# Kernel tuning notes

Hardware: AMD Instinct MI355X
Metric: run time of the kernel (lower is better)

The kernel has to match this reference:

```python
import jax, jax.numpy as jnp
import numpy as np

D_MODEL = 1024
N_HEAD = 16
HEAD_DIM = D_MODEL // N_HEAD
B, S = 4, 2048


def setup_inputs() -> dict:
    key = jax.random.key(0)
    ks = jax.random.split(key, 11)
    scale = 1.0 / np.sqrt(D_MODEL)
    inp = {
        "q": jax.random.normal(ks[0], (B, S, D_MODEL), jnp.float32),
        "k": jax.random.normal(ks[1], (B, S, D_MODEL), jnp.float32),
        "v": jax.random.normal(ks[2], (B, S, D_MODEL), jnp.float32),
        # torch nn.Linear weights: [out_features, in_features], y = x @ W.T + b
        "Wq": jax.random.normal(ks[3], (D_MODEL, D_MODEL), jnp.float32) * scale,
        "bq": jax.random.normal(ks[4], (D_MODEL,), jnp.float32) * scale,
        "Wk": jax.random.normal(ks[5], (D_MODEL, D_MODEL), jnp.float32) * scale,
        "bk": jax.random.normal(ks[6], (D_MODEL,), jnp.float32) * scale,
        "Wv": jax.random.normal(ks[7], (D_MODEL, D_MODEL), jnp.float32) * scale,
        "bv": jax.random.normal(ks[8], (D_MODEL,), jnp.float32) * scale,
        "Wo": jax.random.normal(ks[9], (D_MODEL, D_MODEL), jnp.float32) * scale,
        "bo": jax.random.normal(ks[10], (D_MODEL,), jnp.float32) * scale,
    }
    return inp


def _split_heads(x):
    # [B, S, D] -> [B, H, S, hd]
    b, s, _ = x.shape
    return x.reshape(b, s, N_HEAD, HEAD_DIM).transpose(0, 2, 1, 3)


def reference(q, k, v, Wq, bq, Wk, bk, Wv, bv, Wo, bo):
    qh = _split_heads(q @ Wq.T + bq)
    kh = _split_heads(k @ Wk.T + bk)
    vh = _split_heads(v @ Wv.T + bv)
    scores = jnp.einsum("bhqd,bhkd->bhqk", qh, kh) / jnp.sqrt(
        jnp.asarray(HEAD_DIM, qh.dtype)
    )
    weights = jax.nn.softmax(scores, axis=-1)  # [B, H, Sq, Sk]
    ctx = jnp.einsum("bhqk,bhkd->bhqd", weights, vh)
    b, h, s, d = ctx.shape
    ctx = ctx.transpose(0, 2, 1, 3).reshape(b, s, h * d)  # [B, S, D]
    return ctx @ Wo.T + bo
```

## Files before the change

### kernel.cpp

```cpp
#include <hip/hip_runtime.h>
#include <hip/hip_bf16.h>

typedef float   f32x4   __attribute__((ext_vector_type(4)));
typedef __bf16  bf16x8  __attribute__((ext_vector_type(8)));
typedef unsigned short u16x8 __attribute__((ext_vector_type(8)));
typedef unsigned short u16x4 __attribute__((ext_vector_type(4)));

#define DEVI __device__ __forceinline__

DEVI unsigned short f2bf_bits(float f) {
    __bf16 h = (__bf16)f;
    return __builtin_bit_cast(unsigned short, h);
}

DEVI f32x4 mfma_bf16(bf16x8 a, bf16x8 b, f32x4 c) {
    return __builtin_amdgcn_mfma_f32_16x16x32_bf16(a, b, c, 0, 0, 0);
}

DEVI float fast_exp2(float x) {
#if __has_builtin(__builtin_amdgcn_exp2f)
    return __builtin_amdgcn_exp2f(x);
#else
    float r;
    asm("v_exp_f32 %0, %1" : "=v"(r) : "v"(x));
    return r;
#endif
}

DEVI void gload16(const void* g, void* l) {
    __builtin_amdgcn_global_load_lds(
        (const __attribute__((address_space(1))) void*)g,
        (__attribute__((address_space(3))) void*)l, 16, 0, 0);
}

__global__ __launch_bounds__(256) void convert_w_kernel(
    const float* __restrict__ Wq, const float* __restrict__ Wk,
    const float* __restrict__ Wv, unsigned short* __restrict__ Wb)
{
    int idx = blockIdx.x * 256 + threadIdx.x;
    int which = idx >> 17;
    int off = (idx & 131071) * 8;
    const float* src = which == 0 ? Wq : (which == 1 ? Wk : Wv);
    f32x4 a = *(const f32x4*)(src + off);
    f32x4 b = *(const f32x4*)(src + off + 4);
    u16x8 h;
#pragma unroll
    for (int j = 0; j < 4; ++j) { h[j] = f2bf_bits(a[j]); h[4 + j] = f2bf_bits(b[j]); }
    *(u16x8*)(Wb + (size_t)which * 1048576 + off) = h;
}

template <bool A_ASYNC, bool OUT_F32>
__global__ __launch_bounds__(256) void gemm_bt_kernel(
    const void* __restrict__ Ap, const void* __restrict__ Wp,
    const float* __restrict__ bias, void* __restrict__ Cp,
    int M, int N, int K, float scale)
{
    __shared__ __align__(16) char ldsA[128 * 128];
    __shared__ __align__(16) char ldsB[128 * 128];
    const int t = threadIdx.x;
    const int wave = t >> 6, lane = t & 63;
    const int g = lane >> 4, c = lane & 15;
    const int rowbase = blockIdx.x * 128;
    const int colbase = blockIdx.y * 128;
    const int wr = (wave >> 1) * 64, wc = (wave & 1) * 64;

    const int arow = lane >> 3;
    const int aslot = (lane & 7) ^ arow;

    const float* fbase[4];
#pragma unroll
    for (int ch = 0; ch < 4; ++ch) {
        int id = ch * 256 + t;
        int row = id >> 3;
        int col = (id & 7) * 8;
        if constexpr (A_ASYNC)
            fbase[ch] = (const float*)Wp + (size_t)(colbase + row) * K + col;
        else
            fbase[ch] = (const float*)Ap + (size_t)(rowbase + row) * K + col;
    }

    f32x4 pre0[4], pre1[4];
#pragma unroll
    for (int ch = 0; ch < 4; ++ch) {
        pre0[ch] = *(const f32x4*)(fbase[ch]);
        pre1[ch] = *(const f32x4*)(fbase[ch] + 4);
    }

    f32x4 acc[4][4] = {};

    for (int kt = 0; kt < K; kt += 64) {
        if constexpr (A_ASYNC) {
            const unsigned short* Ab = (const unsigned short*)Ap;
#pragma unroll
            for (int j = 0; j < 4; ++j) {
                int rg = wave * 4 + j;
                int row = rg * 8 + arow;
                gload16(Ab + (size_t)(rowbase + row) * K + kt + aslot * 8,
                        ldsA + rg * 1024);
            }
        } else {
            const unsigned short* Wb = (const unsigned short*)Wp;
#pragma unroll
            for (int j = 0; j < 4; ++j) {
                int rg = wave * 4 + j;
                int row = rg * 8 + arow;
                gload16(Wb + (size_t)(colbase + row) * K + kt + aslot * 8,
                        ldsB + rg * 1024);
            }
        }

#pragma unroll
        for (int ch = 0; ch < 4; ++ch) {
            int id = ch * 256 + t;
            int row = id >> 3;
            int col = (id & 7) * 8;
            int dst = row * 128 + ((col * 2) ^ ((row & 7) << 4));
            u16x8 hv;
#pragma unroll
            for (int j = 0; j < 4; ++j) { hv[j] = f2bf_bits(pre0[ch][j]); hv[4 + j] = f2bf_bits(pre1[ch][j]); }
            if constexpr (A_ASYNC)
                *(u16x8*)(ldsB + dst) = hv;
            else
                *(u16x8*)(ldsA + dst) = hv;
        }
        __syncthreads();

        if (kt + 64 < K) {
#pragma unroll
            for (int ch = 0; ch < 4; ++ch) {
                pre0[ch] = *(const f32x4*)(fbase[ch] + kt + 64);
                pre1[ch] = *(const f32x4*)(fbase[ch] + kt + 68);
            }
        }

#pragma unroll
        for (int kk = 0; kk < 2; ++kk) {
            bf16x8 af[4], bfr[4];
#pragma unroll
            for (int i = 0; i < 4; ++i) {
                int ra = wr + i * 16 + c;
                af[i] = *(const bf16x8*)(ldsA + ra * 128 + ((kk * 64 + g * 16) ^ ((ra & 7) << 4)));
                int rb = wc + i * 16 + c;
                bfr[i] = *(const bf16x8*)(ldsB + rb * 128 + ((kk * 64 + g * 16) ^ ((rb & 7) << 4)));
            }
#pragma unroll
            for (int i = 0; i < 4; ++i)
#pragma unroll
                for (int j = 0; j < 4; ++j)
                    acc[i][j] = mfma_bf16(af[i], bfr[j], acc[i][j]);
        }
        __syncthreads();
    }

#pragma unroll
    for (int j = 0; j < 4; ++j) {
        int coln = colbase + wc + j * 16 + c;
        float bv = bias[coln];
#pragma unroll
        for (int i = 0; i < 4; ++i) {
            int row0 = rowbase + wr + i * 16 + g * 4;
#pragma unroll
            for (int r = 0; r < 4; ++r) {
                float val = (acc[i][j][r] + bv) * scale;
                if constexpr (OUT_F32)
                    ((float*)Cp)[(size_t)(row0 + r) * N + coln] = val;
                else
                    ((unsigned short*)Cp)[(size_t)(row0 + r) * N + coln] = f2bf_bits(val);
            }
        }
    }
}

__global__ __launch_bounds__(256) void transpose_v_kernel(
    const unsigned short* __restrict__ Vp, unsigned short* __restrict__ Vt)
{
    __shared__ unsigned short tile[64][72];
    const int t = threadIdx.x;
    const int bh = blockIdx.y, b = bh >> 4, h = bh & 15;
    const int s0 = blockIdx.x * 64;
#pragma unroll
    for (int ch = 0; ch < 2; ++ch) {
        int id = ch * 256 + t;
        int srow = id >> 3, dcol = (id & 7) * 8;
        u16x8 v = *(const u16x8*)(Vp + (size_t)(b * 2048 + s0 + srow) * 1024 + h * 64 + dcol);
        *(u16x8*)&tile[srow][dcol] = v;
    }
    __syncthreads();
#pragma unroll
    for (int ch = 0; ch < 2; ++ch) {
        int id = ch * 256 + t;
        int drow = id >> 3, scol = (id & 7) * 8;
        u16x8 ov;
#pragma unroll
        for (int j = 0; j < 8; ++j) ov[j] = tile[scol + j][drow];
        *(u16x8*)(Vt + (size_t)(bh * 64 + drow) * 2048 + s0 + scol) = ov;
    }
}

__global__ __launch_bounds__(256) void attn_kernel(
    const unsigned short* __restrict__ Qp, const unsigned short* __restrict__ Kp,
    const unsigned short* __restrict__ Vt, unsigned short* __restrict__ ctx)
{
    __shared__ __align__(16) char ldsK[64 * 128];
    __shared__ __align__(16) char ldsV[64 * 128];
    __shared__ __align__(16) char ldsP[4][4][16 * 128];
    const int t = threadIdx.x;
    const int wave = t >> 6, lane = t & 63;
    const int g = lane >> 4, c = lane & 15;
    const int bh = blockIdx.y, b = bh >> 4, h = bh & 15;
    const int qb = blockIdx.x * 256;

    bf16x8 qf[4][2];
#pragma unroll
    for (int qs = 0; qs < 4; ++qs) {
        const unsigned short* q0 = Qp + (size_t)(b * 2048 + qb + wave * 64 + qs * 16 + c) * 1024 + h * 64;
        qf[qs][0] = *(const bf16x8*)(q0 + 8 * g);
        qf[qs][1] = *(const bf16x8*)(q0 + 32 + 8 * g);
    }

    f32x4 o[4][4] = {};
    float psum[4] = {0.f, 0.f, 0.f, 0.f};

    const int row0 = t >> 3, colB = (t & 7) * 8;
    const int row1 = 32 + row0;
    const int dst0 = row0 * 128 + ((colB * 2) ^ ((row0 & 7) << 4));
    const int dst1 = row1 * 128 + ((colB * 2) ^ ((row1 & 7) << 4));
    const unsigned short* Ksrc = Kp + (size_t)(b * 2048) * 1024 + h * 64;
    const unsigned short* Vsrc = Vt + (size_t)(bh * 64) * 2048;

    u16x8 kv0 = *(const u16x8*)(Ksrc + (size_t)row0 * 1024 + colB);
    u16x8 kv1 = *(const u16x8*)(Ksrc + (size_t)row1 * 1024 + colB);
    u16x8 vv0 = *(const u16x8*)(Vsrc + (size_t)row0 * 2048 + colB);
    u16x8 vv1 = *(const u16x8*)(Vsrc + (size_t)row1 * 2048 + colB);

    for (int kb = 0; kb < 2048; kb += 64) {
        *(u16x8*)(ldsK + dst0) = kv0;
        *(u16x8*)(ldsK + dst1) = kv1;
        *(u16x8*)(ldsV + dst0) = vv0;
        *(u16x8*)(ldsV + dst1) = vv1;
        __syncthreads();

        if (kb + 64 < 2048) {
            kv0 = *(const u16x8*)(Ksrc + (size_t)(kb + 64 + row0) * 1024 + colB);
            kv1 = *(const u16x8*)(Ksrc + (size_t)(kb + 64 + row1) * 1024 + colB);
            vv0 = *(const u16x8*)(Vsrc + (size_t)row0 * 2048 + kb + 64 + colB);
            vv1 = *(const u16x8*)(Vsrc + (size_t)row1 * 2048 + kb + 64 + colB);
        }

        f32x4 s[4][4] = {};
#pragma unroll
        for (int kk = 0; kk < 2; ++kk) {
            bf16x8 kf[4];
#pragma unroll
            for (int ti = 0; ti < 4; ++ti) {
                int rk = ti * 16 + c;
                kf[ti] = *(const bf16x8*)(ldsK + rk * 128 + ((kk * 64 + g * 16) ^ ((rk & 7) << 4)));
            }
#pragma unroll
            for (int qs = 0; qs < 4; ++qs)
#pragma unroll
                for (int ti = 0; ti < 4; ++ti)
                    s[qs][ti] = mfma_bf16(kf[ti], qf[qs][kk], s[qs][ti]);
        }

#pragma unroll
        for (int qs = 0; qs < 4; ++qs) {
            char* pw = ldsP[wave][qs];
#pragma unroll
            for (int ti = 0; ti < 4; ++ti) {
                float p0 = fast_exp2(s[qs][ti][0]);
                float p1 = fast_exp2(s[qs][ti][1]);
                float p2 = fast_exp2(s[qs][ti][2]);
                float p3 = fast_exp2(s[qs][ti][3]);
                psum[qs] += (p0 + p1) + (p2 + p3);
                u16x4 hp;
                hp[0] = f2bf_bits(p0); hp[1] = f2bf_bits(p1);
                hp[2] = f2bf_bits(p2); hp[3] = f2bf_bits(p3);
                *(u16x4*)(pw + c * 128 + ((ti * 32 + g * 8) ^ ((c & 7) << 4))) = hp;
            }
        }

#pragma unroll
        for (int kk = 0; kk < 2; ++kk) {
            bf16x8 vf[4];
#pragma unroll
            for (int ti = 0; ti < 4; ++ti) {
                int rv = ti * 16 + c;
                vf[ti] = *(const bf16x8*)(ldsV + rv * 128 + ((kk * 64 + g * 16) ^ ((rv & 7) << 4)));
            }
#pragma unroll
            for (int qs = 0; qs < 4; ++qs) {
                bf16x8 pa = *(const bf16x8*)(ldsP[wave][qs] + c * 128 + ((kk * 64 + g * 16) ^ ((c & 7) << 4)));
#pragma unroll
                for (int ti = 0; ti < 4; ++ti)
                    o[qs][ti] = mfma_bf16(pa, vf[ti], o[qs][ti]);
            }
        }
        __syncthreads();
    }

#pragma unroll
    for (int qs = 0; qs < 4; ++qs) {
        float ps = psum[qs];
        ps += __shfl_xor(ps, 16);
        ps += __shfl_xor(ps, 32);
#pragma unroll
        for (int r = 0; r < 4; ++r) {
            float inv = 1.0f / __shfl(ps, 4 * g + r);
            int row = qb + wave * 64 + qs * 16 + 4 * g + r;
#pragma unroll
            for (int ti = 0; ti < 4; ++ti) {
                int col = h * 64 + ti * 16 + c;
                ctx[(size_t)(b * 2048 + row) * 1024 + col] = f2bf_bits(o[qs][ti][r] * inv);
            }
        }
    }
}

extern "C" void kernel_launch(void* const* d_in, const int* in_sizes, int n_in,
                              void* d_out, int out_size, void* d_ws, size_t ws_size,
                              hipStream_t stream)
{
    const float* q  = (const float*)d_in[0];
    const float* k  = (const float*)d_in[1];
    const float* v  = (const float*)d_in[2];
    const float* Wq = (const float*)d_in[3];
    const float* bq = (const float*)d_in[4];
    const float* Wk = (const float*)d_in[5];
    const float* bk = (const float*)d_in[6];
    const float* Wv = (const float*)d_in[7];
    const float* bv = (const float*)d_in[8];
    const float* Wo = (const float*)d_in[9];
    const float* bo = (const float*)d_in[10];
    float* out = (float*)d_out;

    char* ws = (char*)d_ws;
    const size_t SZ = (size_t)8192 * 1024 * 2;
    unsigned short* Qp = (unsigned short*)(ws);
    unsigned short* Kp = (unsigned short*)(ws + SZ);
    unsigned short* Vp = (unsigned short*)(ws + 2 * SZ);
    unsigned short* Vt = (unsigned short*)(ws + 3 * SZ);
    unsigned short* ctx = Vp;
    unsigned short* Wbf = Vt;

    const float QSCALE = 0.1803368801111244f;

    convert_w_kernel<<<dim3(1536), 256, 0, stream>>>(Wq, Wk, Wv, Wbf);

    dim3 gg(64, 8);
    gemm_bt_kernel<false, false><<<gg, 256, 0, stream>>>(q, Wbf,           bq, Qp, 8192, 1024, 1024, QSCALE);
    gemm_bt_kernel<false, false><<<gg, 256, 0, stream>>>(k, Wbf + 1048576, bk, Kp, 8192, 1024, 1024, 1.0f);
    gemm_bt_kernel<false, false><<<gg, 256, 0, stream>>>(v, Wbf + 2097152, bv, Vp, 8192, 1024, 1024, 1.0f);
    transpose_v_kernel<<<dim3(32, 64), 256, 0, stream>>>(Vp, Vt);
    attn_kernel<<<dim3(8, 64), 256, 0, stream>>>(Qp, Kp, Vt, ctx);
    gemm_bt_kernel<true, true><<<gg, 256, 0, stream>>>(ctx, Wo, bo, out, 8192, 1024, 1024, 1.0f);
}
```

Before: 224.8 us.

## Use 32x32 MFMA in attention and keep P in registers via permlane swap

Result: slower. 232.0 us (+3.2%).

```diff
diff --git a/kernel.cpp b/kernel.cpp
--- a/kernel.cpp
+++ b/kernel.cpp
@@ -2,9 +2,11 @@
 #include <hip/hip_bf16.h>
 
 typedef float   f32x4   __attribute__((ext_vector_type(4)));
+typedef float   f32x16  __attribute__((ext_vector_type(16)));
 typedef __bf16  bf16x8  __attribute__((ext_vector_type(8)));
 typedef unsigned short u16x8 __attribute__((ext_vector_type(8)));
 typedef unsigned short u16x4 __attribute__((ext_vector_type(4)));
+typedef unsigned int   u32x4v __attribute__((ext_vector_type(4)));
 
 #define DEVI __device__ __forceinline__
 
@@ -15,6 +17,10 @@
 
 DEVI f32x4 mfma_bf16(bf16x8 a, bf16x8 b, f32x4 c) {
     return __builtin_amdgcn_mfma_f32_16x16x32_bf16(a, b, c, 0, 0, 0);
+}
+
+DEVI f32x16 mfma32(bf16x8 a, bf16x8 b, f32x16 c) {
+    return __builtin_amdgcn_mfma_f32_32x32x16_bf16(a, b, c, 0, 0, 0);
 }
 
 DEVI float fast_exp2(float x) {
@@ -27,6 +33,16 @@
 #endif
 }
 
+DEVI unsigned int cvt_pk_bf16(float lo, float hi) {
+    unsigned int r;
+    asm("v_cvt_pk_bf16_f32 %0, %1, %2" : "=v"(r) : "v"(lo), "v"(hi));
+    return r;
+}
+
+DEVI void permlane32_swap(unsigned int& x, unsigned int& y) {
+    asm("v_permlane32_swap_b32 %0, %1" : "+v"(x), "+v"(y));
+}
+
 DEVI void gload16(const void* g, void* l) {
     __builtin_amdgcn_global_load_lds(
         (const __attribute__((address_space(1))) void*)g,
@@ -203,23 +219,22 @@
 {
     __shared__ __align__(16) char ldsK[64 * 128];
     __shared__ __align__(16) char ldsV[64 * 128];
-    __shared__ __align__(16) char ldsP[4][4][16 * 128];
     const int t = threadIdx.x;
     const int wave = t >> 6, lane = t & 63;
-    const int g = lane >> 4, c = lane & 15;
+    const int q32 = lane & 31, hi = lane >> 5;
     const int bh = blockIdx.y, b = bh >> 4, h = bh & 15;
-    const int qb = blockIdx.x * 256;
-
-    bf16x8 qf[4][2];
-#pragma unroll
-    for (int qs = 0; qs < 4; ++qs) {
-        const unsigned short* q0 = Qp + (size_t)(b * 2048 + qb + wave * 64 + qs * 16 + c) * 1024 + h * 64;
-        qf[qs][0] = *(const bf16x8*)(q0 + 8 * g);
-        qf[qs][1] = *(const bf16x8*)(q0 + 32 + 8 * g);
-    }
-
-    f32x4 o[4][4] = {};
-    float psum[4] = {0.f, 0.f, 0.f, 0.f};
+    const int qb = blockIdx.x * 128;
+
+    bf16x8 qf[4];
+    {
+        const unsigned short* qrowp = Qp + (size_t)(b * 2048 + qb + wave * 32 + q32) * 1024 + h * 64;
+#pragma unroll
+        for (int ks = 0; ks < 4; ++ks)
+            qf[ks] = *(const bf16x8*)(qrowp + 16 * ks + 8 * hi);
+    }
+
+    f32x16 o0 = {}, o1 = {};
+    float psum = 0.f;
 
     const int row0 = t >> 3, colB = (t & 7) * 8;
     const int row1 = 32 + row0;
@@ -247,73 +262,63 @@
             vv1 = *(const u16x8*)(Vsrc + (size_t)row1 * 2048 + kb + 64 + colB);
         }
 
-        f32x4 s[4][4] = {};
-#pragma unroll
-        for (int kk = 0; kk < 2; ++kk) {
-            bf16x8 kf[4];
-#pragma unroll
-            for (int ti = 0; ti < 4; ++ti) {
-                int rk = ti * 16 + c;
-                kf[ti] = *(const bf16x8*)(ldsK + rk * 128 + ((kk * 64 + g * 16) ^ ((rk & 7) << 4)));
-            }
-#pragma unroll
-            for (int qs = 0; qs < 4; ++qs)
-#pragma unroll
-                for (int ti = 0; ti < 4; ++ti)
-                    s[qs][ti] = mfma_bf16(kf[ti], qf[qs][kk], s[qs][ti]);
-        }
-
-#pragma unroll
-        for (int qs = 0; qs < 4; ++qs) {
-            char* pw = ldsP[wave][qs];
-#pragma unroll
-            for (int ti = 0; ti < 4; ++ti) {
-                float p0 = fast_exp2(s[qs][ti][0]);
-                float p1 = fast_exp2(s[qs][ti][1]);
-                float p2 = fast_exp2(s[qs][ti][2]);
-                float p3 = fast_exp2(s[qs][ti][3]);
-                psum[qs] += (p0 + p1) + (p2 + p3);
-                u16x4 hp;
-                hp[0] = f2bf_bits(p0); hp[1] = f2bf_bits(p1);
-                hp[2] = f2bf_bits(p2); hp[3] = f2bf_bits(p3);
-                *(u16x4*)(pw + c * 128 + ((ti * 32 + g * 8) ^ ((c & 7) << 4))) = hp;
-            }
-        }
-
-#pragma unroll
-        for (int kk = 0; kk < 2; ++kk) {
-            bf16x8 vf[4];
-#pragma unroll
-            for (int ti = 0; ti < 4; ++ti) {
-                int rv = ti * 16 + c;
-                vf[ti] = *(const bf16x8*)(ldsV + rv * 128 + ((kk * 64 + g * 16) ^ ((rv & 7) << 4)));
-            }
-#pragma unroll
-            for (int qs = 0; qs < 4; ++qs) {
-                bf16x8 pa = *(const bf16x8*)(ldsP[wave][qs] + c * 128 + ((kk * 64 + g * 16) ^ ((c & 7) << 4)));
-#pragma unroll
-                for (int ti = 0; ti < 4; ++ti)
-                    o[qs][ti] = mfma_bf16(pa, vf[ti], o[qs][ti]);
-            }
+        f32x16 s0 = {}, s1 = {};
+#pragma unroll
+        for (int ks = 0; ks < 4; ++ks) {
+            int rk0 = q32;
+            bf16x8 kf0 = *(const bf16x8*)(ldsK + rk0 * 128 + ((ks * 32 + 16 * hi) ^ ((rk0 & 7) << 4)));
+            s0 = mfma32(kf0, qf[ks], s0);
+            int rk1 = 32 + q32;
+            bf16x8 kf1 = *(const bf16x8*)(ldsK + rk1 * 128 + ((ks * 32 + 16 * hi) ^ ((rk1 & 7) << 4)));
+            s1 = mfma32(kf1, qf[ks], s1);
+        }
+
+#pragma unroll
+        for (int r = 0; r < 16; ++r) { s0[r] = fast_exp2(s0[r]); psum += s0[r]; }
+#pragma unroll
+        for (int r = 0; r < 16; ++r) { s1[r] = fast_exp2(s1[r]); psum += s1[r]; }
+
+#pragma unroll
+        for (int ks = 0; ks < 4; ++ks) {
+            int r0 = (ks & 1) * 8;
+            unsigned int x0, x1, y0, y1;
+            if (ks < 2) {
+                x0 = cvt_pk_bf16(s0[r0],     s0[r0 + 1]);
+                x1 = cvt_pk_bf16(s0[r0 + 2], s0[r0 + 3]);
+                y0 = cvt_pk_bf16(s0[r0 + 4], s0[r0 + 5]);
+                y1 = cvt_pk_bf16(s0[r0 + 6], s0[r0 + 7]);
+            } else {
+                x0 = cvt_pk_bf16(s1[r0],     s1[r0 + 1]);
+                x1 = cvt_pk_bf16(s1[r0 + 2], s1[r0 + 3]);
+                y0 = cvt_pk_bf16(s1[r0 + 4], s1[r0 + 5]);
+                y1 = cvt_pk_bf16(s1[r0 + 6], s1[r0 + 7]);
+            }
+            permlane32_swap(x0, y0);
+            permlane32_swap(x1, y1);
+            u32x4v pw; pw[0] = x0; pw[1] = x1; pw[2] = y0; pw[3] = y1;
+            bf16x8 pa = __builtin_bit_cast(bf16x8, pw);
+
+            int rv0 = q32;
+            bf16x8 vf0 = *(const bf16x8*)(ldsV + rv0 * 128 + ((ks * 32 + 16 * hi) ^ ((rv0 & 7) << 4)));
+            o0 = mfma32(pa, vf0, o0);
+            int rv1 = 32 + q32;
+            bf16x8 vf1 = *(const bf16x8*)(ldsV + rv1 * 128 + ((ks * 32 + 16 * hi) ^ ((rv1 & 7) << 4)));
+            o1 = mfma32(pa, vf1, o1);
         }
         __syncthreads();
     }
 
-#pragma unroll
-    for (int qs = 0; qs < 4; ++qs) {
-        float ps = psum[qs];
-        ps += __shfl_xor(ps, 16);
-        ps += __shfl_xor(ps, 32);
-#pragma unroll
-        for (int r = 0; r < 4; ++r) {
-            float inv = 1.0f / __shfl(ps, 4 * g + r);
-            int row = qb + wave * 64 + qs * 16 + 4 * g + r;
-#pragma unroll
-            for (int ti = 0; ti < 4; ++ti) {
-                int col = h * 64 + ti * 16 + c;
-                ctx[(size_t)(b * 2048 + row) * 1024 + col] = f2bf_bits(o[qs][ti][r] * inv);
-            }
-        }
+    psum += __shfl_xor(psum, 32);
+    float invown = 1.0f / psum;
+
+#pragma unroll
+    for (int r = 0; r < 16; ++r) {
+        int rowl = (r & 3) + 8 * (r >> 2) + 4 * hi;
+        float inv = __shfl(invown, rowl);
+        int row = qb + wave * 32 + rowl;
+        size_t base = (size_t)(b * 2048 + row) * 1024 + h * 64;
+        ctx[base + q32]      = f2bf_bits(o0[r] * inv);
+        ctx[base + 32 + q32] = f2bf_bits(o1[r] * inv);
     }
 }
 
@@ -352,6 +357,6 @@
     gemm_bt_kernel<false, false><<<gg, 256, 0, stream>>>(k, Wbf + 1048576, bk, Kp, 8192, 1024, 1024, 1.0f);
     gemm_bt_kernel<false, false><<<gg, 256, 0, stream>>>(v, Wbf + 2097152, bv, Vp, 8192, 1024, 1024, 1.0f);
     transpose_v_kernel<<<dim3(32, 64), 256, 0, stream>>>(Vp, Vt);
-    attn_kernel<<<dim3(8, 64), 256, 0, stream>>>(Qp, Kp, Vt, ctx);
+    attn_kernel<<<dim3(16, 64), 256, 0, stream>>>(Qp, Kp, Vt, ctx);
     gemm_bt_kernel<true, true><<<gg, 256, 0, stream>>>(ctx, Wo, bo, out, 8192, 1024, 1024, 1.0f);
 }
```
